# Kernel optimization log

Hardware: AMD Instinct MI355X
Metric: run time of the kernel (lower is better)

The kernel has to match this reference:

```python
import jax, jax.numpy as jnp
import numpy as np


def _pos_encoding(seq_len, d_model, dtype):
    # Faithful to the original: exponent uses dim itself (not dim-1 for odd dims).
    dims = jnp.arange(d_model, dtype=dtype)                     # [D]
    positions = jnp.arange(seq_len, dtype=dtype)                # [S]
    inv_freq = jnp.power(jnp.asarray(10000.0, dtype), dims / d_model)  # [D]
    angle = positions[:, None] / inv_freq[None, :]              # [S, D]
    even = (jnp.arange(d_model) % 2) == 0                       # [D]
    return jnp.where(even[None, :], jnp.sin(angle), jnp.cos(angle))  # [S, D]


def setup_inputs() -> dict:
    key = jax.random.key(0)
    x = jax.random.normal(key, (8, 4096, 1024), dtype=jnp.float32)
    return {"x": x}


def reference(x) -> jnp.ndarray:
    B, S, D = x.shape
    enc = _pos_encoding(S, D, x.dtype)  # [S, D]
    # Dropout in eval mode is identity, so output is x + encoding.
    return x + enc[None, :, :]
```

## Files before the change

kernel.cpp:

```cpp
#include <hip/hip_runtime.h>
#include <hip/hip_bf16.h>
#include <math.h>


#define S_LEN 4096
#define D_LEN 1024

__global__ __launch_bounds__(256) void pe_add_kernel(
    const float* __restrict__ x, float* __restrict__ out, int B) {
    const int s   = blockIdx.x;
    const int tid = threadIdx.x;
    const int d0  = tid << 2;

    const float sf = (float)s;
    const float c = -9.210340371976184f / (float)D_LEN;

    float enc0, enc1, enc2, enc3;
    {
        float a0 = sf * expf((float)(d0 + 0) * c);
        float a1 = sf * expf((float)(d0 + 1) * c);
        float a2 = sf * expf((float)(d0 + 2) * c);
        float a3 = sf * expf((float)(d0 + 3) * c);
        enc0 = sinf(a0);
        enc1 = cosf(a1);
        enc2 = sinf(a2);
        enc3 = cosf(a3);
    }

    size_t base = (size_t)s * D_LEN + (size_t)d0;
    const size_t bstride = (size_t)S_LEN * D_LEN;

    #pragma unroll
    for (int b = 0; b < 8; ++b) {
        if (b >= B) break;
        const float4* px = (const float4*)(x + base + (size_t)b * bstride);
        float4 v = *px;
        v.x += enc0;
        v.y += enc1;
        v.z += enc2;
        v.w += enc3;
        *(float4*)(out + base + (size_t)b * bstride) = v;
    }
}

extern "C" void kernel_launch(void* const* d_in, const int* in_sizes, int n_in,
                              void* d_out, int out_size, void* d_ws, size_t ws_size,
                              hipStream_t stream) {
    const float* x = (const float*)d_in[0];
    float* out = (float*)d_out;
    const int B = in_sizes[0] / (S_LEN * D_LEN);

    dim3 grid(S_LEN);
    dim3 block(D_LEN / 4);
    pe_add_kernel<<<grid, block, 0, stream>>>(x, out, B);
}
```

Baseline: 230.1 us.

## Precompute encoding table in workspace and add with per-batch blocks

Computes the sinusoidal encoding once into a workspace buffer with a separate kernel, then launches one block per (batch, position) pair to add it to x with nontemporal stores. This raises the number of independent blocks and memory requests in flight compared with one block looping over the batch. In exchange it adds a second launch and extra traffic for writing and re-reading the encoding table. A fallback keeps the old fused path when the workspace is too small or the batch is not 8.

```diff
diff --git a/kernel.cpp b/kernel.cpp
--- a/kernel.cpp
+++ b/kernel.cpp
@@ -1,12 +1,48 @@
 #include <hip/hip_runtime.h>
-#include <hip/hip_bf16.h>
 #include <math.h>
 
 
 #define S_LEN 4096
 #define D_LEN 1024
 
-__global__ __launch_bounds__(256) void pe_add_kernel(
+typedef float f32x4 __attribute__((ext_vector_type(4)));
+
+__global__ __launch_bounds__(256) void enc_kernel(float* __restrict__ enc) {
+    const int s  = blockIdx.x;
+    const int d0 = threadIdx.x << 2;
+
+    const float sf = (float)s;
+    const float c = -9.210340371976184f / (float)D_LEN;
+
+    const float a0 = sf * expf((float)(d0 + 0) * c);
+    const float a1 = sf * expf((float)(d0 + 1) * c);
+    const float a2 = sf * expf((float)(d0 + 2) * c);
+    const float a3 = sf * expf((float)(d0 + 3) * c);
+    f32x4 e;
+    e.x = sinf(a0);
+    e.y = cosf(a1);
+    e.z = sinf(a2);
+    e.w = cosf(a3);
+
+    *(f32x4*)(enc + (size_t)s * D_LEN + d0) = e;
+}
+
+__global__ __launch_bounds__(256) void add_kernel(
+    const float* __restrict__ x, const float* __restrict__ enc,
+    float* __restrict__ out) {
+    const int b = blockIdx.x & 7;
+    const int s = blockIdx.x >> 3;
+
+    const size_t row = (size_t)s * D_LEN + ((size_t)threadIdx.x << 2);
+    const size_t off = (size_t)b * ((size_t)S_LEN * D_LEN) + row;
+
+    f32x4 e = *(const f32x4*)(enc + row);
+    f32x4 v = *(const f32x4*)(x + off);
+    v += e;
+    __builtin_nontemporal_store(v, (f32x4*)(out + off));
+}
+
+__global__ __launch_bounds__(256) void pe_add_fallback(
     const float* __restrict__ x, float* __restrict__ out, int B) {
     const int s   = blockIdx.x;
     const int tid = threadIdx.x;
@@ -30,9 +66,7 @@
     size_t base = (size_t)s * D_LEN + (size_t)d0;
     const size_t bstride = (size_t)S_LEN * D_LEN;
 
-    #pragma unroll
-    for (int b = 0; b < 8; ++b) {
-        if (b >= B) break;
+    for (int b = 0; b < B; ++b) {
         const float4* px = (const float4*)(x + base + (size_t)b * bstride);
         float4 v = *px;
         v.x += enc0;
@@ -50,7 +84,13 @@
     float* out = (float*)d_out;
     const int B = in_sizes[0] / (S_LEN * D_LEN);
 
-    dim3 grid(S_LEN);
-    dim3 block(D_LEN / 4);
-    pe_add_kernel<<<grid, block, 0, stream>>>(x, out, B);
+    const size_t enc_bytes = (size_t)S_LEN * D_LEN * sizeof(float);
+
+    if (B == 8 && d_ws != nullptr && ws_size >= enc_bytes) {
+        float* enc = (float*)d_ws;
+        enc_kernel<<<dim3(S_LEN), dim3(D_LEN / 4), 0, stream>>>(enc);
+        add_kernel<<<dim3(S_LEN * 8), dim3(D_LEN / 4), 0, stream>>>(x, enc, out);
+    } else {
+        pe_add_fallback<<<dim3(S_LEN), dim3(D_LEN / 4), 0, stream>>>(x, out, B);
+    }
 }
```

Result: slower. 240.3 us (+4.4%).

## Flatten grid to strided float4 walk with nontemporal stores and two-row encoding reuse

Applied to the files above, without the earlier changes.

Launches half as many blocks and has each thread walk the flattened tensor with a fixed stride, so each thread covers two sequence rows across all batches and reuses two precomputed encoding vectors. Output writes use nontemporal stores to avoid polluting the cache on a pure streaming workload, and the loop is unrolled to keep several loads in flight. A generic fallback loop handles batch sizes other than 8. The main cost targeted is memory bandwidth efficiency; the exchange is fewer resident waves and a specialised fast path tied to B=8.

```diff
diff --git a/kernel.cpp b/kernel.cpp
--- a/kernel.cpp
+++ b/kernel.cpp
@@ -1,45 +1,68 @@
 #include <hip/hip_runtime.h>
-#include <hip/hip_bf16.h>
 #include <math.h>
 
 
 #define S_LEN 4096
 #define D_LEN 1024
 
+typedef float f32x4 __attribute__((ext_vector_type(4)));
+
+#define NF4_ROW   256
+#define TSTRIDE   (2048 * 256)
+#define NITER     16
+
 __global__ __launch_bounds__(256) void pe_add_kernel(
     const float* __restrict__ x, float* __restrict__ out, int B) {
-    const int s   = blockIdx.x;
-    const int tid = threadIdx.x;
-    const int d0  = tid << 2;
+    const int t = blockIdx.x * 256 + threadIdx.x;
 
-    const float sf = (float)s;
     const float c = -9.210340371976184f / (float)D_LEN;
 
-    float enc0, enc1, enc2, enc3;
-    {
-        float a0 = sf * expf((float)(d0 + 0) * c);
-        float a1 = sf * expf((float)(d0 + 1) * c);
-        float a2 = sf * expf((float)(d0 + 2) * c);
-        float a3 = sf * expf((float)(d0 + 3) * c);
-        enc0 = sinf(a0);
-        enc1 = cosf(a1);
-        enc2 = sinf(a2);
-        enc3 = cosf(a3);
-    }
+    if (B == 8) {
+        const int col = t & (NF4_ROW - 1);
+        const int r0  = t >> 8;
+        const int d0  = col << 2;
 
-    size_t base = (size_t)s * D_LEN + (size_t)d0;
-    const size_t bstride = (size_t)S_LEN * D_LEN;
+        const float f0 = expf((float)(d0 + 0) * c);
+        const float f1 = expf((float)(d0 + 1) * c);
+        const float f2 = expf((float)(d0 + 2) * c);
+        const float f3 = expf((float)(d0 + 3) * c);
 
-    #pragma unroll
-    for (int b = 0; b < 8; ++b) {
-        if (b >= B) break;
-        const float4* px = (const float4*)(x + base + (size_t)b * bstride);
-        float4 v = *px;
-        v.x += enc0;
-        v.y += enc1;
-        v.z += enc2;
-        v.w += enc3;
-        *(float4*)(out + base + (size_t)b * bstride) = v;
+        const float sa = (float)r0;
+        const float sb = (float)(r0 + 2048);
+
+        f32x4 ea, eb;
+        ea.x = sinf(sa * f0); ea.y = cosf(sa * f1);
+        ea.z = sinf(sa * f2); ea.w = cosf(sa * f3);
+        eb.x = sinf(sb * f0); eb.y = cosf(sb * f1);
+        eb.z = sinf(sb * f2); eb.w = cosf(sb * f3);
+
+        const f32x4* px = (const f32x4*)x + t;
+        f32x4*       po = (f32x4*)out + t;
+
+        #pragma unroll 4
+        for (int k = 0; k < NITER; ++k) {
+            f32x4 v = *px;
+            v += (k & 1) ? eb : ea;
+            __builtin_nontemporal_store(v, po);
+            px += TSTRIDE;
+            po += TSTRIDE;
+        }
+    } else {
+        const size_t nf4 = (size_t)B * S_LEN * (D_LEN / 4);
+        for (size_t i = t; i < nf4; i += (size_t)TSTRIDE) {
+            const int col = (int)(i & (NF4_ROW - 1));
+            const int s   = (int)((i / NF4_ROW) % S_LEN);
+            const int d0  = col << 2;
+            const float sf = (float)s;
+            f32x4 e;
+            e.x = sinf(sf * expf((float)(d0 + 0) * c));
+            e.y = cosf(sf * expf((float)(d0 + 1) * c));
+            e.z = sinf(sf * expf((float)(d0 + 2) * c));
+            e.w = cosf(sf * expf((float)(d0 + 3) * c));
+            f32x4 v = ((const f32x4*)x)[i];
+            v += e;
+            ((f32x4*)out)[i] = v;
+        }
     }
 }
 
@@ -50,7 +73,7 @@
     float* out = (float*)d_out;
     const int B = in_sizes[0] / (S_LEN * D_LEN);
 
-    dim3 grid(S_LEN);
-    dim3 block(D_LEN / 4);
+    dim3 grid(2048);
+    dim3 block(256);
     pe_add_kernel<<<grid, block, 0, stream>>>(x, out, B);
 }
```

Result: slower. 235.2 us (+2.2%).
